# Optimization experiments

Hardware: AMD Instinct MI355X
Metric: run time of the kernel (lower is better)

Reference implementation:

```python
import jax, jax.numpy as jnp
import numpy as np
from jax import lax

DATA_NUM, CNUM, AUG_NUM, LNUM = 64, 6, 4, 3
B, H, W = 16, 512, 512
T_SEL = 0  # fixed aug selection (torch draws np.random.randint at runtime)
EPS = 1e-8
DN = ('NCHW', 'OIHW', 'NCHW')


def setup_inputs() -> dict:
    key = jax.random.key(0)
    ks = jax.random.split(key, 8)
    GLA_img_aug = jax.random.uniform(ks[0], (B, 1, H, W), dtype=jnp.float32)
    lbl = jax.random.randint(ks[1], (B, H, W), 0, CNUM, dtype=jnp.int32)
    index = jax.random.randint(ks[2], (B,), 0, DATA_NUM, dtype=jnp.int32)
    # learned params: Bezier control params (5+2=7 slots, only 0..3 used) and per-(sample,class,aug,layer) tiny conv pairs
    param = jax.random.uniform(ks[3], (DATA_NUM, CNUM, AUG_NUM, LNUM, 7), dtype=jnp.float32)
    w1 = 0.1 * jax.random.normal(ks[4], (DATA_NUM, CNUM, AUG_NUM, LNUM, 4, 1, 3, 3), dtype=jnp.float32)
    b1 = 0.01 * jax.random.normal(ks[5], (DATA_NUM, CNUM, AUG_NUM, LNUM, 4), dtype=jnp.float32)
    w2 = 0.1 * jax.random.normal(ks[6], (DATA_NUM, CNUM, AUG_NUM, LNUM, 1, 4, 3, 3), dtype=jnp.float32)
    b2 = 0.01 * jax.random.normal(ks[7], (DATA_NUM, CNUM, AUG_NUM, LNUM, 1), dtype=jnp.float32)
    return {"GLA_img_aug": GLA_img_aug, "lbl": lbl, "index": index,
            "param": param, "w1": w1, "b1": b1, "w2": w2, "b2": b2}


def _conv_pair(x, w1, b1, w2, b2):
    # x: [1,H,W]; per-sample Conv2d(1,4,3,p=1) -> Conv2d(4,1,3,p=1)
    y = lax.conv_general_dilated(x[None], w1, (1, 1), 'SAME', dimension_numbers=DN) + b1[None, :, None, None]
    y = lax.conv_general_dilated(y, w2, (1, 1), 'SAME', dimension_numbers=DN) + b2[None, :, None, None]
    return y[0]

_conv_batch = jax.vmap(_conv_pair)  # batched over per-sample weights


def _ftransfer(xn, lbl, i, index, param, w1, b1, w2, b2):
    raw = xn                                   # [B,1,H,W]
    mask = (lbl[:, None, :, :] == i)           # [B,1,H,W]
    c = xn * mask
    pp = jax.nn.sigmoid(param[index, i, T_SEL])   # [B,L,7]  (p := sigmoid)
    W1, B1 = w1[index, i, T_SEL], b1[index, i, T_SEL]
    W2, B2 = w2[index, i, T_SEL], b2[index, i, T_SEL]
    for layer in range(LNUM):
        p1 = pp[:, layer, 0][:, None, None, None]
        p2 = pp[:, layer, 1][:, None, None, None]
        p1v = pp[:, layer, 2][:, None, None, None]
        p2v = pp[:, layer, 3][:, None, None, None]
        mix = jax.nn.sigmoid(_conv_batch(raw, W1[:, layer], B1[:, layer], W2[:, layer], B2[:, layer]))
        om = 1.0 - c
        ct = 3.0 * om**2 * c * p1 + 3.0 * om * c**2 * p2 + c**3          # p0=0,  p3=1
        cv = om**3 + 3.0 * om**2 * c * p1v + 3.0 * om * c**2 * p2v       # p0v=1, p3v=0
        c = jnp.clip(ct * mix + cv * (1.0 - mix), 0.0, 1.0)
    # write back only where label == i (equivalent to torch's flag-filtered scatter)
    return jnp.where(mask, c, raw)


def reference(GLA_img_aug, lbl, index, param, w1, b1, w2, b2):
    x = GLA_img_aug
    mn = jnp.min(x, axis=(1, 2, 3), keepdims=True)
    mx = jnp.max(x, axis=(1, 2, 3), keepdims=True)
    scale = mx - mn + EPS
    xn = (x - mn) / scale
    for i in range(CNUM):
        xn = _ftransfer(xn, lbl, i, index, param, w1, b1, w2, b2)
    return xn * scale + mn
```

## Files before the change

### kernel.cpp

```cpp
#include <hip/hip_runtime.h>
#include <stdint.h>

#define HW 512
#define IMG (HW*HW)
#define CNUM_ 6

#define TILE 64
#define HALO 12
#define ST 88
#define SSTR 89
#define NT 512
#define RCAP 256

typedef float f2 __attribute__((ext_vector_type(2)));

#define LTOT 3840

#define RECBASE 1024
#define REC_F 96
#define VARBASE (RECBASE + 96*REC_F)
#define VAR_F 27

__global__ __launch_bounds__(256) void k_prep(const float4* __restrict__ x4,
                       const int* __restrict__ index, const float* __restrict__ param,
                       const float* __restrict__ w1, const float* __restrict__ b1,
                       const float* __restrict__ w2, const float* __restrict__ b2,
                       float* __restrict__ wsf){
    __shared__ float w1s[108], w2s[108], b1s[12], b2s[3], prm[21];
    __shared__ float smn[4], smx[4];
    const int r = blockIdx.x, t = threadIdx.x;
    if (r >= 96){
        int blk = r - 96;
        int base4 = blk * 4096;
        float vmin = 1e30f, vmax = -1e30f;
#pragma unroll
        for (int k = 0; k < 16; k++){
            float4 v = x4[base4 + k*256 + t];
            vmin = fminf(vmin, fminf(fminf(v.x, v.y), fminf(v.z, v.w)));
            vmax = fmaxf(vmax, fmaxf(fmaxf(v.x, v.y), fmaxf(v.z, v.w)));
        }
#pragma unroll
        for (int off = 32; off > 0; off >>= 1){
            vmin = fminf(vmin, __shfl_down(vmin, off));
            vmax = fmaxf(vmax, __shfl_down(vmax, off));
        }
        int wv = t >> 6;
        if ((t & 63) == 0){ smn[wv] = vmin; smx[wv] = vmax; }
        __syncthreads();
        if (t == 0){
            wsf[2*blk]     = fminf(fminf(smn[0], smn[1]), fminf(smn[2], smn[3]));
            wsf[2*blk + 1] = fmaxf(fmaxf(smx[0], smx[1]), fmaxf(smx[2], smx[3]));
        }
        return;
    }
    const int b = r / 6, i = r % 6;
    const int lb0 = (index[b]*CNUM_ + i) * 12;
    if (t < 108){
        int l = t / 36, j = t % 36;
        w1s[t] = w1[(lb0 + l)*36 + j];
        w2s[t] = w2[(lb0 + l)*36 + j];
    }
    if (t < 12) b1s[t] = b1[(lb0 + t/4)*4 + (t%4)];
    if (t < 3)  b2s[t] = b2[lb0 + t];
    if (t < 21) prm[t] = param[(lb0 + t/7)*7 + (t%7)];
    __syncthreads();
    float* rec = wsf + RECBASE + r*REC_F;
    float* var = wsf + VARBASE + r*9*3*VAR_F;
    for (int u = t; u < 9*3*26; u += 256){
        int kind = u / 78, rem = u % 78, l = rem / 26, e = rem % 26;
        int rowk = kind / 3, colk = kind % 3;
        if (e < 25){
            int ty = e/5 - 2, tx = e%5 - 2;
            float we = 0.f;
            for (int d = 0; d < 9; d++){
                int dy = d/3 - 1, dx = d%3 - 1;
                if ((rowk==0 && dy<0)||(rowk==2 && dy>0)||(colk==0 && dx<0)||(colk==2 && dx>0)) continue;
                int ey = ty - dy, ex = tx - dx;
                if (ey < -1 || ey > 1 || ex < -1 || ex > 1) continue;
                for (int c = 0; c < 4; c++)
                    we += w2s[l*36 + c*9 + d] * w1s[l*36 + c*9 + (ey+1)*3 + (ex+1)];
            }
            var[(kind*3 + l)*VAR_F + e] = we;
            if (kind == 4) rec[l*25 + e] = we;
        } else {
            float be = b2s[l];
            for (int c = 0; c < 4; c++){
                float sw = 0.f;
                for (int d = 0; d < 9; d++){
                    int dy = d/3 - 1, dx = d%3 - 1;
                    if ((rowk==0 && dy<0)||(rowk==2 && dy>0)||(colk==0 && dx<0)||(colk==2 && dx>0)) continue;
                    sw += w2s[l*36 + c*9 + d];
                }
                be += b1s[l*4 + c] * sw;
            }
            var[(kind*3 + l)*VAR_F + 25] = be;
            if (kind == 4) rec[75 + l] = be;
        }
    }
    if (t < 18){
        int l = t / 6, q = t % 6;
        float p1  = __builtin_amdgcn_rcpf(1.f + __expf(-prm[l*7 + 0]));
        float p2  = __builtin_amdgcn_rcpf(1.f + __expf(-prm[l*7 + 1]));
        float p1v = __builtin_amdgcn_rcpf(1.f + __expf(-prm[l*7 + 2]));
        float p2v = __builtin_amdgcn_rcpf(1.f + __expf(-prm[l*7 + 3]));
        float v;
        switch (q){
            case 0: v = 3.f*p1; break;
            case 1: v = 3.f*p2 - 6.f*p1; break;
            case 2: v = 1.f + 3.f*p1 - 3.f*p2; break;
            case 3: v = 3.f*p1v - 3.f; break;
            case 4: v = 3.f - 6.f*p1v + 3.f*p2v; break;
            default: v = -1.f + 3.f*p1v - 3.f*p2v; break;
        }
        rec[78 + l*6 + q] = v;
    }
}

__device__ __forceinline__ float sig1(float z){
    return __builtin_amdgcn_rcpf(1.f + __expf(-z));
}

__device__ __forceinline__ float bez3(float c, float mix, const float* __restrict__ cf){
    float ct = c * (cf[0] + c * (cf[1] + c * cf[2]));
    float cv = 1.f + c * (cf[3] + c * (cf[4] + c * cf[5]));
    float r = cv + mix * (ct - cv);
    return __builtin_amdgcn_fmed3f(r, 0.f, 1.f);
}

__device__ __forceinline__ f2 splat(float v){ f2 r = {v, v}; return r; }

__device__ __forceinline__ f2 sig2(f2 z){
    f2 r;
    r.x = __builtin_amdgcn_rcpf(1.f + __expf(-z.x));
    r.y = __builtin_amdgcn_rcpf(1.f + __expf(-z.y));
    return r;
}

__device__ __forceinline__ f2 bez3p(f2 c, f2 mix, const float* __restrict__ cf){
    f2 ct = c * (splat(cf[0]) + c * (splat(cf[1]) + c * splat(cf[2])));
    f2 cv = splat(1.f) + c * (splat(cf[3]) + c * (splat(cf[4]) + c * splat(cf[5])));
    f2 r = cv + mix * (ct - cv);
    r.x = __builtin_amdgcn_fmed3f(r.x, 0.f, 1.f);
    r.y = __builtin_amdgcn_fmed3f(r.y, 0.f, 1.f);
    return r;
}

__device__ __forceinline__ void load_taps(const float* __restrict__ s, int pos, float* tp){
    const volatile float* sp0 = s + pos - (2*SSTR + 2);
    const volatile float* sp1 = s + pos + (SSTR - 2);
#pragma unroll
    for (int wy = 0; wy < 3; wy++)
#pragma unroll
    for (int wx = 0; wx < 5; wx++)
        tp[wy*5 + wx] = sp0[wy*SSTR + wx];
#pragma unroll
    for (int wy = 0; wy < 2; wy++)
#pragma unroll
    for (int wx = 0; wx < 5; wx++)
        tp[15 + wy*5 + wx] = sp1[wy*SSTR + wx];
}

__device__ __forceinline__ void conv_px(const float* __restrict__ s, int pos,
                                        const float* __restrict__ rec,
                                        float& z0, float& z1, float& z2, float& cc){
    float tp[25];
    load_taps(s, pos, tp);
    f2 a0 = {rec[75], 0.f};
    f2 a1 = {rec[76], 0.f};
    f2 a2 = {rec[77], 0.f};
#pragma unroll
    for (int e = 0; e < 24; e += 2){
        f2 tv = {tp[e], tp[e+1]};
        f2 w0 = {rec[e],      rec[e+1]};
        f2 w1 = {rec[25 + e], rec[26 + e]};
        f2 w2 = {rec[50 + e], rec[51 + e]};
        a0 += w0 * tv;
        a1 += w1 * tv;
        a2 += w2 * tv;
    }
    float t24 = tp[24];
    z0 = a0.x + a0.y + rec[24]*t24;
    z1 = a1.x + a1.y + rec[49]*t24;
    z2 = a2.x + a2.y + rec[74]*t24;
    cc = tp[12];
}

__device__ __forceinline__ unsigned short* gl_addr(float* out, int sbase, int Y0, int X0, int e){
    return (unsigned short*)(out + sbase + (Y0 + HALO + (e >> 7))*HW + X0 + HALO) + (e & 127);
}

__global__ __launch_bounds__(NT, 8) void k_main(
        const float* __restrict__ x, const int* __restrict__ lbl,
        float* __restrict__ out, const float* __restrict__ wsf){
    __shared__ float s[ST*SSTR];
    __shared__ unsigned short lst[LTOT];
    __shared__ unsigned rlst[RCAP];
    __shared__ int cnt[8];
    __shared__ float snorm[4];
    const int lin = ((blockIdx.z << 3) + blockIdx.y) * 8 + blockIdx.x;
    const int tile = ((lin & 7) << 7) + (lin >> 3);
    const int bz = tile >> 6, by = (tile >> 3) & 7, bx = tile & 7;
    const int b = bz;
    const int X0 = bx * TILE - HALO, Y0 = by * TILE - HALO;
    const int tid = threadIdx.x;
    const int lane = tid & 63;
    const int sbase = b * IMG;
    const bool edgeblk = (bx == 0) | (bx == 7) | (by == 0) | (by == 7);

    if (tid < 8) cnt[tid] = 0;
    if (tid < 16){
        float pmn = wsf[2*(b*16 + tid)];
        float pmx = wsf[2*(b*16 + tid) + 1];
#pragma unroll
        for (int off = 8; off > 0; off >>= 1){
            pmn = fminf(pmn, __shfl_down(pmn, off));
            pmx = fmaxf(pmx, __shfl_down(pmx, off));
        }
        if (tid == 0){
            float scv = pmx - pmn + 1e-8f;
            snorm[0] = pmn; snorm[1] = scv; snorm[2] = 1.0f / scv;
        }
    }
    __syncthreads();
    const float mn = snorm[0], sc = snorm[1], inv = snorm[2];
    const float mninv = mn * inv;

#define ADV(yy, xx) { int w_ = (xx) + (NT % ST); int f_ = (w_ >= ST); \
                      (xx) = w_ - (f_ ? ST : 0); (yy) += (NT/ST) + f_; }
#define LOADPX(yy, xx, vv, cc) { \
        int cy_ = min(max(Y0 + (yy), 0), HW-1); \
        int cx_ = min(max(X0 + (xx), 0), HW-1); \
        int o_ = sbase + cy_*HW + cx_; \
        vv = x[o_]; cc = lbl[o_]; }

    int y0c = tid / ST, x0c = tid % ST;
    int y1c = y0c, x1c = x0c; ADV(y1c, x1c);
    int y2c = y1c, x2c = x1c; ADV(y2c, x2c);
    float vA, vB, vC; int cA, cB, cC;
    LOADPX(y0c, x0c, vA, cA);
    LOADPX(y1c, x1c, vB, cB);
    LOADPX(y2c, x2c, vC, cC);

#pragma unroll
    for (int it = 0; it < 16; it++){
        const int ly = y0c, lx = x0c;
        const bool inb = (it < 15) || (tid < ST*ST - 15*NT);
        const int gy = Y0 + ly, gx = X0 + lx;
        const bool valid = inb && (unsigned)gy < (unsigned)HW && (unsigned)gx < (unsigned)HW;
        const float v = valid ? (vA*inv - mninv) : 0.f;
        const int c = valid ? cA : 255;
        if (inb) s[ly*SSTR + lx] = v;
        int margin = min(min(lx, ST-1-lx), min(ly, ST-1-ly));
        bool ring = valid && ((gx==0) | (gx==HW-1) | (gy==0) | (gy==HW-1));
        bool mainok = valid && !ring && c < CNUM_ && margin >= 2 + 2*c;
        int ce = mainok ? c : 7;
        unsigned short pos = (unsigned short)(ly*SSTR + lx);

        y0c = y1c; x0c = x1c; y1c = y2c; x1c = x2c;
        vA = vB; cA = cB; vB = vC; cB = cC;
        ADV(y2c, x2c);
        if (it <= 12) LOADPX(y2c, x2c, vC, cC);

        unsigned long long m0 = __ballot(ce & 1);
        unsigned long long m1 = __ballot(ce & 2);
        unsigned long long m2 = __ballot(ce & 4);
        int basev = 0;
        if (lane < 6){
            unsigned long long mc = ((lane & 1) ? m0 : ~m0)
                                  & ((lane & 2) ? m1 : ~m1)
                                  & ((lane & 4) ? m2 : ~m2);
            int pc = __popcll(mc);
            if (pc) basev = atomicAdd(&cnt[lane], pc);
        }
        int mybase = __shfl(basev, ce < 6 ? ce : 0);
        if (mainok){
            unsigned long long mself = ((ce & 1) ? m0 : ~m0)
                                     & ((ce & 2) ? m1 : ~m1)
                                     & ((ce & 4) ? m2 : ~m2);
            int p = mybase + __popcll(mself & ((1ull << lane) - 1ull));
            if (ce < 3){
                int capc = 1408 - (ce << 7);
                int offc = ce * (1472 - (ce << 6));
                if (p < capc) lst[offc + p] = pos;
            } else {
                int d = ce - 3;
                int capc = 1056 - 96*d;
                int offc = d * (1104 - 48*d);
                if (p < capc) *gl_addr(out, sbase, Y0, X0, offc + p) = pos;
            }
        }
        if (edgeblk){
            bool ringok = ring && c < CNUM_ && margin >= 2;
            unsigned long long rm = __ballot(ringok);
            if (rm){
                int base = 0;
                if (lane == 0) base = atomicAdd(&cnt[6], __popcll(rm));
                base = __shfl(base, 0);
                if (ringok){
                    int p = base + __popcll(rm & ((1ull << lane) - 1ull));
                    if (p < RCAP) rlst[p] = ((unsigned)c << 16) | pos;
                }
            }
        }
    }
#undef ADV
#undef LOADPX
    __syncthreads();
    const int rn = min(cnt[6], RCAP);

    unsigned short pf[9];
#pragma unroll
    for (int d = 0; d < 3; d++){
        int capc = 1056 - 96*d;
        int offc = d * (1104 - 48*d);
        int nB = min(cnt[3 + d], capc);
#pragma unroll
        for (int sl = 0; sl < 3; sl++){
            int j = tid + sl*NT;
            unsigned short pv = 0;
            if (j < nB) pv = *gl_addr(out, sbase, Y0, X0, offc + j);
            pf[d*3 + sl] = pv;
        }
    }

#pragma unroll
    for (int cls = 0; cls < CNUM_; cls++){
        const int capc = (cls < 3) ? (1408 - (cls << 7)) : (1056 - 96*(cls - 3));
        const float* rec = wsf + RECBASE + (b*CNUM_ + cls)*REC_F;
        const int n = min(cnt[cls], capc);
        const int j0 = tid, j1 = tid + NT, j2 = tid + 2*NT;
        const bool v0 = j0 < n, v1 = j1 < n, v2 = j2 < n;
        int p0 = 0, p1 = 0, p2 = 0;
        if (cls < 3){
            const unsigned short* lp = lst + cls * (1472 - (cls << 6));
            if (v0) p0 = lp[j0];
            if (v1) p1 = lp[j1];
            if (v2) p2 = lp[j2];
        } else {
            p0 = pf[(cls-3)*3 + 0];
            p1 = pf[(cls-3)*3 + 1];
            p2 = pf[(cls-3)*3 + 2];
        }
        float z00=0.f, z01=0.f, z02=0.f, cc0=0.f;
        float z10=0.f, z11=0.f, z12=0.f, cc1=0.f;
        float u0, u1, u2;
        if (v0) conv_px(s, p0, rec, z00, z01, z02, cc0);
        if (v1) conv_px(s, p1, rec, z10, z11, z12, cc1);
        if (v0 | v1){
            f2 cP = {cc0, cc1};
            cP = bez3p(cP, sig2((f2){z00, z10}), rec + 78);
            cP = bez3p(cP, sig2((f2){z01, z11}), rec + 84);
            cP = bez3p(cP, sig2((f2){z02, z12}), rec + 90);
            u0 = cP.x; u1 = cP.y;
        }
        if (v2){
            float za, zb, zc, cc;
            conv_px(s, p2, rec, za, zb, zc, cc);
            cc = bez3(cc, sig1(za), rec + 78);
            cc = bez3(cc, sig1(zb), rec + 84);
            u2 = bez3(cc, sig1(zc), rec + 90);
        }
        int hav = -1; float rupd = 0.f;
        if (edgeblk && tid < rn){
            unsigned e = rlst[tid];
            int rc = (int)(e >> 16), pos = (int)(e & 0xffff);
            int ly = pos / SSTR, lx = pos % SSTR;
            int margin = min(min(lx, ST-1-lx), min(ly, ST-1-ly));
            if (rc == cls && margin >= 2 + 2*cls){
                int gy = Y0 + ly, gx = X0 + lx;
                int rowk = (gy == 0) ? 0 : ((gy == HW-1) ? 2 : 1);
                int colk = (gx == 0) ? 0 : ((gx == HW-1) ? 2 : 1);
                const float* vb = wsf + VARBASE + ((b*CNUM_ + cls)*9 + rowk*3 + colk)*3*VAR_F;
                float tp[25];
                load_taps(s, pos, tp);
                float c = tp[12];
#pragma unroll
                for (int l = 0; l < 3; l++){
                    float z = vb[l*VAR_F + 25];
#pragma unroll
                    for (int e2 = 0; e2 < 25; e2++) z += vb[l*VAR_F + e2] * tp[e2];
                    c = bez3(c, sig1(z), rec + 78 + 6*l);
                }
                rupd = c; hav = pos;
            }
        }
        __syncthreads();
        if (v0) s[p0] = u0;
        if (v1) s[p1] = u1;
        if (v2) s[p2] = u2;
        if (hav >= 0) s[hav] = rupd;
        __syncthreads();
    }

    for (int j = tid; j < TILE*TILE; j += NT){
        int py = j >> 6, px = j & 63;
        int gy = Y0 + HALO + py, gx = X0 + HALO + px;
        out[sbase + gy*HW + gx] = s[(HALO + py)*SSTR + (HALO + px)] * sc + mn;
    }
}

extern "C" void kernel_launch(void* const* d_in, const int* in_sizes, int n_in,
                              void* d_out, int out_size, void* d_ws, size_t ws_size,
                              hipStream_t stream){
    const float* x     = (const float*)d_in[0];
    const int*   lbl   = (const int*)  d_in[1];
    const int*   index = (const int*)  d_in[2];
    const float* param = (const float*)d_in[3];
    const float* w1    = (const float*)d_in[4];
    const float* b1    = (const float*)d_in[5];
    const float* w2    = (const float*)d_in[6];
    const float* b2    = (const float*)d_in[7];
    float* out = (float*)d_out;
    float* wsf = (float*)d_ws;

    k_prep<<<352, 256, 0, stream>>>((const float4*)x, index, param, w1, b1, w2, b2, wsf);
    dim3 g(8, 8, 16);
    k_main<<<g, NT, 0, stream>>>(x, lbl, out, wsf);
}
```

Measured before the change: 174.0 us.

## Drop volatile tap loads, simplify tile fill, hoist list and ring decoding

Removes the volatile qualifier on the shared-memory tap loads so the compiler can merge and schedule LDS reads. Replaces the software-pipelined, fully unrolled tile-fill loop with a simple indexed loop that loads pixels directly. Precomputes the clamped per-class counts, the class 0-2 position lists and the ring-pixel decode once before the class loop, so that per-class work is only the compute. This trades register pressure and the lost prefetch of global loads for fewer redundant LDS reads and integer divisions.

```diff
diff --git a/kernel.cpp b/kernel.cpp
--- a/kernel.cpp
+++ b/kernel.cpp
@@ -146,8 +146,8 @@
 }
 
 __device__ __forceinline__ void load_taps(const float* __restrict__ s, int pos, float* tp){
-    const volatile float* sp0 = s + pos - (2*SSTR + 2);
-    const volatile float* sp1 = s + pos + (SSTR - 2);
+    const float* sp0 = s + pos - (2*SSTR + 2);
+    const float* sp1 = s + pos + (SSTR - 2);
 #pragma unroll
     for (int wy = 0; wy < 3; wy++)
 #pragma unroll
@@ -225,41 +225,24 @@
     const float mn = snorm[0], sc = snorm[1], inv = snorm[2];
     const float mninv = mn * inv;
 
-#define ADV(yy, xx) { int w_ = (xx) + (NT % ST); int f_ = (w_ >= ST); \
-                      (xx) = w_ - (f_ ? ST : 0); (yy) += (NT/ST) + f_; }
-#define LOADPX(yy, xx, vv, cc) { \
-        int cy_ = min(max(Y0 + (yy), 0), HW-1); \
-        int cx_ = min(max(X0 + (xx), 0), HW-1); \
-        int o_ = sbase + cy_*HW + cx_; \
-        vv = x[o_]; cc = lbl[o_]; }
-
-    int y0c = tid / ST, x0c = tid % ST;
-    int y1c = y0c, x1c = x0c; ADV(y1c, x1c);
-    int y2c = y1c, x2c = x1c; ADV(y2c, x2c);
-    float vA, vB, vC; int cA, cB, cC;
-    LOADPX(y0c, x0c, vA, cA);
-    LOADPX(y1c, x1c, vB, cB);
-    LOADPX(y2c, x2c, vC, cC);
-
-#pragma unroll
     for (int it = 0; it < 16; it++){
-        const int ly = y0c, lx = x0c;
-        const bool inb = (it < 15) || (tid < ST*ST - 15*NT);
-        const int gy = Y0 + ly, gx = X0 + lx;
-        const bool valid = inb && (unsigned)gy < (unsigned)HW && (unsigned)gx < (unsigned)HW;
-        const float v = valid ? (vA*inv - mninv) : 0.f;
-        const int c = valid ? cA : 255;
+        int k = it*NT + tid;
+        bool inb = k < ST*ST;
+        int ly = k / ST, lx = k % ST;
+        int gy = Y0 + ly, gx = X0 + lx;
+        bool valid = inb && (unsigned)gy < (unsigned)HW && (unsigned)gx < (unsigned)HW;
+        float v = 0.f; int c = 255;
+        if (valid){
+            int off = sbase + gy*HW + gx;
+            v = x[off]*inv - mninv;
+            c = lbl[off];
+        }
         if (inb) s[ly*SSTR + lx] = v;
         int margin = min(min(lx, ST-1-lx), min(ly, ST-1-ly));
         bool ring = valid && ((gx==0) | (gx==HW-1) | (gy==0) | (gy==HW-1));
         bool mainok = valid && !ring && c < CNUM_ && margin >= 2 + 2*c;
         int ce = mainok ? c : 7;
         unsigned short pos = (unsigned short)(ly*SSTR + lx);
-
-        y0c = y1c; x0c = x1c; y1c = y2c; x1c = x2c;
-        vA = vB; cA = cB; vB = vC; cB = cC;
-        ADV(y2c, x2c);
-        if (it <= 12) LOADPX(y2c, x2c, vC, cC);
 
         unsigned long long m0 = __ballot(ce & 1);
         unsigned long long m1 = __ballot(ce & 2);
@@ -303,43 +286,55 @@
             }
         }
     }
-#undef ADV
-#undef LOADPX
     __syncthreads();
+
+    int ncnt[6];
+#pragma unroll
+    for (int cc6 = 0; cc6 < 6; cc6++)
+        ncnt[cc6] = min(cnt[cc6], (cc6 < 3) ? (1408 - (cc6 << 7)) : (1056 - 96*(cc6 - 3)));
     const int rn = min(cnt[6], RCAP);
 
+    unsigned short pl[9];
+#pragma unroll
+    for (int c3 = 0; c3 < 3; c3++){
+        const unsigned short* lp = lst + c3 * (1472 - (c3 << 6));
+        const int n = ncnt[c3];
+        pl[c3*3+0] = (tid        < n) ? lp[tid]        : (unsigned short)0;
+        pl[c3*3+1] = (tid +   NT < n) ? lp[tid +   NT] : (unsigned short)0;
+        pl[c3*3+2] = (tid + 2*NT < n) ? lp[tid + 2*NT] : (unsigned short)0;
+    }
     unsigned short pf[9];
 #pragma unroll
     for (int d = 0; d < 3; d++){
-        int capc = 1056 - 96*d;
         int offc = d * (1104 - 48*d);
-        int nB = min(cnt[3 + d], capc);
+        int nB = ncnt[3 + d];
 #pragma unroll
         for (int sl = 0; sl < 3; sl++){
             int j = tid + sl*NT;
-            unsigned short pv = 0;
-            if (j < nB) pv = *gl_addr(out, sbase, Y0, X0, offc + j);
-            pf[d*3 + sl] = pv;
-        }
+            pf[d*3 + sl] = (j < nB) ? *gl_addr(out, sbase, Y0, X0, offc + j) : (unsigned short)0;
+        }
+    }
+    int rpos = -1, rcls = 8, rrowk = 1, rcolk = 1, rmarg = 0;
+    if (edgeblk && tid < rn){
+        unsigned e = rlst[tid];
+        rcls = (int)(e >> 16); rpos = (int)(e & 0xffff);
+        int ly = rpos / SSTR, lx = rpos % SSTR;
+        rmarg = min(min(lx, ST-1-lx), min(ly, ST-1-ly));
+        int gy = Y0 + ly, gx = X0 + lx;
+        rrowk = (gy == 0) ? 0 : ((gy == HW-1) ? 2 : 1);
+        rcolk = (gx == 0) ? 0 : ((gx == HW-1) ? 2 : 1);
     }
 
 #pragma unroll
     for (int cls = 0; cls < CNUM_; cls++){
-        const int capc = (cls < 3) ? (1408 - (cls << 7)) : (1056 - 96*(cls - 3));
         const float* rec = wsf + RECBASE + (b*CNUM_ + cls)*REC_F;
-        const int n = min(cnt[cls], capc);
-        const int j0 = tid, j1 = tid + NT, j2 = tid + 2*NT;
-        const bool v0 = j0 < n, v1 = j1 < n, v2 = j2 < n;
-        int p0 = 0, p1 = 0, p2 = 0;
+        const int n = ncnt[cls];
+        const bool v0 = tid < n, v1 = tid + NT < n, v2 = tid + 2*NT < n;
+        int p0, p1, p2;
         if (cls < 3){
-            const unsigned short* lp = lst + cls * (1472 - (cls << 6));
-            if (v0) p0 = lp[j0];
-            if (v1) p1 = lp[j1];
-            if (v2) p2 = lp[j2];
+            p0 = pl[cls*3 + 0]; p1 = pl[cls*3 + 1]; p2 = pl[cls*3 + 2];
         } else {
-            p0 = pf[(cls-3)*3 + 0];
-            p1 = pf[(cls-3)*3 + 1];
-            p2 = pf[(cls-3)*3 + 2];
+            p0 = pf[(cls-3)*3 + 0]; p1 = pf[(cls-3)*3 + 1]; p2 = pf[(cls-3)*3 + 2];
         }
         float z00=0.f, z01=0.f, z02=0.f, cc0=0.f;
         float z10=0.f, z11=0.f, z12=0.f, cc1=0.f;
@@ -361,28 +356,19 @@
             u2 = bez3(cc, sig1(zc), rec + 90);
         }
         int hav = -1; float rupd = 0.f;
-        if (edgeblk && tid < rn){
-            unsigned e = rlst[tid];
-            int rc = (int)(e >> 16), pos = (int)(e & 0xffff);
-            int ly = pos / SSTR, lx = pos % SSTR;
-            int margin = min(min(lx, ST-1-lx), min(ly, ST-1-ly));
-            if (rc == cls && margin >= 2 + 2*cls){
-                int gy = Y0 + ly, gx = X0 + lx;
-                int rowk = (gy == 0) ? 0 : ((gy == HW-1) ? 2 : 1);
-                int colk = (gx == 0) ? 0 : ((gx == HW-1) ? 2 : 1);
-                const float* vb = wsf + VARBASE + ((b*CNUM_ + cls)*9 + rowk*3 + colk)*3*VAR_F;
-                float tp[25];
-                load_taps(s, pos, tp);
-                float c = tp[12];
-#pragma unroll
-                for (int l = 0; l < 3; l++){
-                    float z = vb[l*VAR_F + 25];
-#pragma unroll
-                    for (int e2 = 0; e2 < 25; e2++) z += vb[l*VAR_F + e2] * tp[e2];
-                    c = bez3(c, sig1(z), rec + 78 + 6*l);
-                }
-                rupd = c; hav = pos;
+        if (rcls == cls && rmarg >= 2 + 2*cls){
+            const float* vb = wsf + VARBASE + ((b*CNUM_ + cls)*9 + rrowk*3 + rcolk)*3*VAR_F;
+            float tp[25];
+            load_taps(s, rpos, tp);
+            float c = tp[12];
+#pragma unroll
+            for (int l = 0; l < 3; l++){
+                float z = vb[l*VAR_F + 25];
+#pragma unroll
+                for (int e2 = 0; e2 < 25; e2++) z += vb[l*VAR_F + e2] * tp[e2];
+                c = bez3(c, sig1(z), rec + 78 + 6*l);
             }
+            rupd = c; hav = rpos;
         }
         __syncthreads();
         if (v0) s[p0] = u0;
```

Result: faster. 166.2 us (-4.4%).
